# Optimization experiments

Hardware: AMD Instinct MI355X
Metric: run time of the kernel (lower is better)

The kernel has to match this reference:

```python
import jax, jax.numpy as jnp
import numpy as np

NUM_EXPERTS = 8
TOP_K = 2
HIDDEN = 1024
INTER = 1408


def setup_inputs() -> dict:
    key = jax.random.key(0)
    k0, k1, k2, k3, k4 = jax.random.split(key, 5)
    B, S = 2, 2048
    d_scale = HIDDEN ** -0.5
    i_scale = INTER ** -0.5
    return {
        "hidden_states": jax.random.normal(k0, (B, S, HIDDEN), jnp.float32),
        # nn.Linear(hidden, num_experts, bias=False): weight (E, d)
        "gate_w": jax.random.normal(k1, (NUM_EXPERTS, HIDDEN), jnp.float32) * d_scale,
        # per-expert SwiGLU weights, nn.Linear convention (out, in)
        "gate_proj": jax.random.normal(k2, (NUM_EXPERTS, INTER, HIDDEN), jnp.float32) * d_scale,
        "up_proj": jax.random.normal(k3, (NUM_EXPERTS, INTER, HIDDEN), jnp.float32) * d_scale,
        "down_proj": jax.random.normal(k4, (NUM_EXPERTS, HIDDEN, INTER), jnp.float32) * i_scale,
    }


def reference(hidden_states, gate_w, gate_proj, up_proj, down_proj):
    B, S, D = hidden_states.shape
    x = hidden_states.reshape(-1, D)  # (T, d)
    T = x.shape[0]

    # gate linear -> router logits (T, E)
    router_logits = x @ gate_w.T

    # TopKRouter: softmax in fp32 over all experts, top-k, optional renorm
    probs = jax.nn.softmax(router_logits.astype(jnp.float32), axis=-1)
    routing_weights, selected_experts = jax.lax.top_k(probs, TOP_K)  # (T, k)
    routing_weights = routing_weights / routing_weights.sum(axis=-1, keepdims=True)  # norm_topk_prob
    routing_weights = routing_weights.astype(x.dtype)

    # combine weights per (token, expert): scatter top-k weights into dense (T, E)
    combine = jnp.zeros((T, NUM_EXPERTS), x.dtype).at[
        jnp.arange(T)[:, None], selected_experts
    ].add(routing_weights)

    # per-expert SwiGLU FFN, weighted combine (loop over small fixed expert set)
    out = jnp.zeros_like(x)
    for e in range(NUM_EXPERTS):
        h = jax.nn.silu(x @ gate_proj[e].T) * (x @ up_proj[e].T)  # (T, i)
        out = out + combine[:, e : e + 1] * (h @ down_proj[e].T)  # (T, d)

    return out.reshape(B, S, D), router_logits
```

## Files before the change

kernel.cpp:

```cpp
#include <hip/hip_runtime.h>
#include <hip/hip_bf16.h>
#include <stdint.h>

#define T_TOK 4096
#define DH 1024
#define DI 1408
#define NE 8
#define TOPK 2
#define PADROWS 9216

typedef short s16x8 __attribute__((ext_vector_type(8)));
typedef float f32x4 __attribute__((ext_vector_type(4)));

__device__ inline unsigned f2bf(float f) {
    __hip_bfloat16 h = __float2bfloat16(f);
    return (unsigned)*(unsigned short*)&h;
}

__global__ __launch_bounds__(256) void cvt3_kernel(const float* __restrict__ s0,
        const float* __restrict__ s1, const float* __restrict__ s2,
        unsigned short* __restrict__ t0, unsigned short* __restrict__ t1,
        unsigned short* __restrict__ t2, int n4) {
    const float* src = blockIdx.y == 0 ? s0 : (blockIdx.y == 1 ? s1 : s2);
    unsigned short* dst = blockIdx.y == 0 ? t0 : (blockIdx.y == 1 ? t1 : t2);
    int i = blockIdx.x * blockDim.x + threadIdx.x;
    int stride = gridDim.x * blockDim.x;
    for (; i < n4; i += stride) {
        float4 v = ((const float4*)src)[i];
        uint2 o;
        o.x = f2bf(v.x) | (f2bf(v.y) << 16);
        o.y = f2bf(v.z) | (f2bf(v.w) << 16);
        ((uint2*)dst)[i] = o;
    }
}

__global__ __launch_bounds__(256) void router_kernel(const float* __restrict__ x,
                              const float* __restrict__ gw,
                              float* __restrict__ logits_out,
                              int* __restrict__ tokE, float* __restrict__ tokW,
                              unsigned short* __restrict__ xb) {
    int wave = threadIdx.x >> 6;
    int lane = threadIdx.x & 63;
    int t = blockIdx.x * 4 + wave;
    const float4* xr = (const float4*)(x + (size_t)t * DH);

    float acc[NE];
#pragma unroll
    for (int e = 0; e < NE; ++e) acc[e] = 0.f;

#pragma unroll
    for (int i = 0; i < 4; ++i) {
        float4 xv = xr[lane + i * 64];
#pragma unroll
        for (int e = 0; e < NE; ++e) {
            float4 g = ((const float4*)(gw + (size_t)e * DH))[lane + i * 64];
            acc[e] += xv.x * g.x + xv.y * g.y + xv.z * g.z + xv.w * g.w;
        }
        uint2 o;
        o.x = f2bf(xv.x) | (f2bf(xv.y) << 16);
        o.y = f2bf(xv.z) | (f2bf(xv.w) << 16);
        *(uint2*)(xb + (size_t)t * DH + (lane + i * 64) * 4) = o;
    }
#pragma unroll
    for (int e = 0; e < NE; ++e) {
#pragma unroll
        for (int off = 32; off > 0; off >>= 1) acc[e] += __shfl_xor(acc[e], off, 64);
    }
    if (lane == 0) {
        float mx = acc[0];
#pragma unroll
        for (int e = 1; e < NE; ++e) mx = fmaxf(mx, acc[e]);
        float p[NE]; float s = 0.f;
#pragma unroll
        for (int e = 0; e < NE; ++e) { p[e] = expf(acc[e] - mx); s += p[e]; }
        float inv = 1.f / s;
#pragma unroll
        for (int e = 0; e < NE; ++e) p[e] *= inv;
        int i0 = 0, i1 = -1; float p0 = -1.f, p1 = -1.f;
#pragma unroll
        for (int e = 0; e < NE; ++e) {
            float v = p[e];
            if (v > p0) { p1 = p0; i1 = i0; p0 = v; i0 = e; }
            else if (v > p1) { p1 = v; i1 = e; }
        }
        float wsum = p0 + p1;
#pragma unroll
        for (int e = 0; e < NE; ++e) logits_out[(size_t)t * NE + e] = acc[e];
        tokE[2 * t]     = i0;  tokE[2 * t + 1] = i1;
        tokW[2 * t]     = p0 / wsum;  tokW[2 * t + 1] = p1 / wsum;
    }
}

__global__ __launch_bounds__(256) void hist_kernel(const int* __restrict__ tokE,
        int* __restrict__ counts, int* __restrict__ padOff) {
    __shared__ int wc[4][NE];
    int tid = threadIdx.x;
    int wave = tid >> 6, lane = tid & 63;
    int cnt[NE];
#pragma unroll
    for (int e = 0; e < NE; ++e) cnt[e] = 0;
    for (int i = tid; i < T_TOK * TOPK; i += 256) {
        int v = tokE[i];
#pragma unroll
        for (int e = 0; e < NE; ++e)
            cnt[e] += (int)__popcll(__ballot(v == e));
    }
    if (lane == 0) {
#pragma unroll
        for (int e = 0; e < NE; ++e) wc[wave][e] = cnt[e];
    }
    __syncthreads();
    if (tid == 0) {
        int r = 0;
        for (int e = 0; e < NE; ++e) {
            int c = wc[0][e] + wc[1][e] + wc[2][e] + wc[3][e];
            counts[e] = c;
            padOff[e] = r;
            r += ((c + 127) >> 7) << 7;
        }
        padOff[NE] = r;
    }
}

__global__ __launch_bounds__(256) void scatter_kernel(const int* __restrict__ tokE,
                               const int* __restrict__ padOff, int* __restrict__ cursor,
                               int* __restrict__ assignTok, int* __restrict__ tokSlot) {
    int t = blockIdx.x * blockDim.x + threadIdx.x;
    int lane = threadIdx.x & 63;
    unsigned long long lmask = (1ull << lane) - 1ull;
#pragma unroll
    for (int k = 0; k < TOPK; ++k) {
        int e = tokE[2 * t + k];
#pragma unroll
        for (int ex = 0; ex < NE; ++ex) {
            unsigned long long m = __ballot(e == ex);
            if (e == ex) {
                int rank = (int)__popcll(m & lmask);
                int leader = __ffsll((long long)m) - 1;
                int b = 0;
                if (rank == 0) b = atomicAdd(&cursor[ex], (int)__popcll(m));
                b = __shfl(b, leader, 64);
                int slot = padOff[ex] + b + rank;
                assignTok[slot] = t;
                tokSlot[2 * t + k] = slot;
            }
        }
    }
}

__global__ __launch_bounds__(512) void gemmA_kernel(
        const unsigned short* __restrict__ xb,
        const unsigned short* __restrict__ gpb, const unsigned short* __restrict__ upb,
        const int* __restrict__ padOff, const int* __restrict__ assignTok,
        unsigned short* __restrict__ h) {
    int pr0 = blockIdx.y * 128;
    int e = -1;
#pragma unroll
    for (int i = 0; i < NE; ++i)
        if (pr0 >= padOff[i] && pr0 < padOff[i + 1]) e = i;
    if (e < 0) return;
    int n0 = blockIdx.x * 128;

    __shared__ unsigned short As[128 * 32];
    __shared__ unsigned short Bgs[128 * 32];
    __shared__ unsigned short Bus[128 * 32];

    int tid = threadIdx.x;
    int lane = tid & 63;
    int w = tid >> 6;
    int wm = (w >> 2) * 64;
    int wn = (w & 3) * 32;

    int tok = assignTok[pr0 + w * 16 + (lane >> 2)];
    const unsigned short* a_src = xb + (size_t)tok * DH + (lane & 3) * 8;
    unsigned short* a_dst = &As[w * 16 * 32];

    int brow = n0 + w * 16 + (lane >> 2);
    const unsigned short* g_src = gpb + ((size_t)e * DI + brow) * DH + (lane & 3) * 8;
    const unsigned short* u_src = upb + ((size_t)e * DI + brow) * DH + (lane & 3) * 8;
    unsigned short* bg_dst = &Bgs[w * 16 * 32];
    unsigned short* bu_dst = &Bus[w * 16 * 32];

    f32x4 accG[4][2], accU[4][2];
#pragma unroll
    for (int i = 0; i < 4; ++i)
#pragma unroll
        for (int j = 0; j < 2; ++j) {
            accG[i][j] = (f32x4){0.f, 0.f, 0.f, 0.f};
            accU[i][j] = (f32x4){0.f, 0.f, 0.f, 0.f};
        }

    for (int k0 = 0; k0 < DH; k0 += 32) {
        __builtin_amdgcn_global_load_lds(
            (const __attribute__((address_space(1))) void*)(a_src + k0),
            (__attribute__((address_space(3))) void*)a_dst, 16, 0, 0);
        __builtin_amdgcn_global_load_lds(
            (const __attribute__((address_space(1))) void*)(g_src + k0),
            (__attribute__((address_space(3))) void*)bg_dst, 16, 0, 0);
        __builtin_amdgcn_global_load_lds(
            (const __attribute__((address_space(1))) void*)(u_src + k0),
            (__attribute__((address_space(3))) void*)bu_dst, 16, 0, 0);
        __syncthreads();

        s16x8 af[4], bgf[2], buf_[2];
#pragma unroll
        for (int i = 0; i < 4; ++i)
            af[i] = *(const s16x8*)&As[(wm + 16 * i + (lane & 15)) * 32 + (lane >> 4) * 8];
#pragma unroll
        for (int j = 0; j < 2; ++j) {
            bgf[j]  = *(const s16x8*)&Bgs[(wn + 16 * j + (lane & 15)) * 32 + (lane >> 4) * 8];
            buf_[j] = *(const s16x8*)&Bus[(wn + 16 * j + (lane & 15)) * 32 + (lane >> 4) * 8];
        }
#pragma unroll
        for (int i = 0; i < 4; ++i)
#pragma unroll
            for (int j = 0; j < 2; ++j) {
                accG[i][j] = __builtin_amdgcn_mfma_f32_16x16x32_bf16(af[i], bgf[j], accG[i][j], 0, 0, 0);
                accU[i][j] = __builtin_amdgcn_mfma_f32_16x16x32_bf16(af[i], buf_[j], accU[i][j], 0, 0, 0);
            }
        __syncthreads();
    }

#pragma unroll
    for (int i = 0; i < 4; ++i) {
        int rowb = pr0 + wm + 16 * i + ((lane >> 4) << 2);
#pragma unroll
        for (int j = 0; j < 2; ++j) {
            int col = n0 + wn + 16 * j + (lane & 15);
#pragma unroll
            for (int r = 0; r < 4; ++r) {
                float g = accG[i][j][r], u = accU[i][j][r];
                float val = (g / (1.f + __expf(-g))) * u;
                h[(size_t)(rowb + r) * DI + col] = (unsigned short)f2bf(val);
            }
        }
    }
}

__global__ __launch_bounds__(512) void gemmB_kernel(
        const unsigned short* __restrict__ h,
        const unsigned short* __restrict__ dpb,
        const int* __restrict__ padOff, const int* __restrict__ counts,
        float* __restrict__ outP) {
    int pr0 = blockIdx.y * 128;
    int e = -1, base = 0;
#pragma unroll
    for (int i = 0; i < NE; ++i)
        if (pr0 >= padOff[i] && pr0 < padOff[i + 1]) { e = i; base = padOff[i]; }
    if (e < 0) return;
    int cnt = counts[e];
    int n0 = blockIdx.x * 128;

    __shared__ unsigned short As[128 * 32];
    __shared__ unsigned short Bs[128 * 32];

    int tid = threadIdx.x;
    int lane = tid & 63;
    int w = tid >> 6;
    int wm = (w >> 2) * 64;
    int wn = (w & 3) * 32;

    const unsigned short* a_src = h + (size_t)(pr0 + w * 16 + (lane >> 2)) * DI + (lane & 3) * 8;
    unsigned short* a_dst = &As[w * 16 * 32];

    int brow = n0 + w * 16 + (lane >> 2);
    const unsigned short* b_src = dpb + ((size_t)e * DH + brow) * DI + (lane & 3) * 8;
    unsigned short* b_dst = &Bs[w * 16 * 32];

    f32x4 acc[4][2];
#pragma unroll
    for (int i = 0; i < 4; ++i)
#pragma unroll
        for (int j = 0; j < 2; ++j) acc[i][j] = (f32x4){0.f, 0.f, 0.f, 0.f};

    for (int k0 = 0; k0 < DI; k0 += 32) {
        __builtin_amdgcn_global_load_lds(
            (const __attribute__((address_space(1))) void*)(a_src + k0),
            (__attribute__((address_space(3))) void*)a_dst, 16, 0, 0);
        __builtin_amdgcn_global_load_lds(
            (const __attribute__((address_space(1))) void*)(b_src + k0),
            (__attribute__((address_space(3))) void*)b_dst, 16, 0, 0);
        __syncthreads();

        s16x8 af[4], bf[2];
#pragma unroll
        for (int i = 0; i < 4; ++i)
            af[i] = *(const s16x8*)&As[(wm + 16 * i + (lane & 15)) * 32 + (lane >> 4) * 8];
#pragma unroll
        for (int j = 0; j < 2; ++j)
            bf[j] = *(const s16x8*)&Bs[(wn + 16 * j + (lane & 15)) * 32 + (lane >> 4) * 8];
#pragma unroll
        for (int i = 0; i < 4; ++i)
#pragma unroll
            for (int j = 0; j < 2; ++j)
                acc[i][j] = __builtin_amdgcn_mfma_f32_16x16x32_bf16(af[i], bf[j], acc[i][j], 0, 0, 0);
        __syncthreads();
    }

#pragma unroll
    for (int i = 0; i < 4; ++i) {
        int rowb = pr0 + wm + 16 * i + ((lane >> 4) << 2);
#pragma unroll
        for (int r = 0; r < 4; ++r) {
            int prow = rowb + r;
            if (prow - base < cnt) {
#pragma unroll
                for (int j = 0; j < 2; ++j) {
                    int col = n0 + wn + 16 * j + (lane & 15);
                    outP[(size_t)prow * DH + col] = acc[i][j][r];
                }
            }
        }
    }
}

__global__ __launch_bounds__(256) void combine_kernel(const float* __restrict__ outP,
        const int* __restrict__ tokSlot, const float* __restrict__ tokW,
        float* __restrict__ out) {
    int t = blockIdx.x;
    int c = threadIdx.x * 4;
    int s0 = tokSlot[2 * t], s1 = tokSlot[2 * t + 1];
    float w0 = tokW[2 * t], w1 = tokW[2 * t + 1];
    float4 a = *(const float4*)(outP + (size_t)s0 * DH + c);
    float4 b = *(const float4*)(outP + (size_t)s1 * DH + c);
    float4 o;
    o.x = w0 * a.x + w1 * b.x;
    o.y = w0 * a.y + w1 * b.y;
    o.z = w0 * a.z + w1 * b.z;
    o.w = w0 * a.w + w1 * b.w;
    *(float4*)(out + (size_t)t * DH + c) = o;
}

extern "C" void kernel_launch(void* const* d_in, const int* in_sizes, int n_in,
                              void* d_out, int out_size, void* d_ws, size_t ws_size,
                              hipStream_t stream) {
    const float* x  = (const float*)d_in[0];
    const float* gw = (const float*)d_in[1];
    const float* gp = (const float*)d_in[2];
    const float* up = (const float*)d_in[3];
    const float* dp = (const float*)d_in[4];
    float* out = (float*)d_out;
    float* logits = out + (size_t)T_TOK * DH;

    char* ws = (char*)d_ws;
    int*   counts    = (int*)(ws + 0);
    int*   cursor    = (int*)(ws + 64);
    int*   padOff    = (int*)(ws + 128);
    int*   tokE      = (int*)(ws + 4096);
    float* tokW      = (float*)(ws + 36864);
    int*   tokSlot   = (int*)(ws + 69632);
    int*   assignTok = (int*)(ws + 102400);
    unsigned short* xb  = (unsigned short*)(ws + 139264);
    unsigned short* gpb = (unsigned short*)(ws + 8527872);
    unsigned short* upb = (unsigned short*)(ws + 31596544);
    unsigned short* dpb = (unsigned short*)(ws + 54665216);
    unsigned short* h   = (unsigned short*)(ws + 77733888);
    float* outP = (float*)(ws + 8527872);

    hipMemsetAsync(ws, 0, 256, stream);
    hipMemsetAsync(ws + 102400, 0, PADROWS * 4, stream);

    const int NW4 = NE * DI * DH / 4;
    cvt3_kernel<<<dim3(1024, 3), 256, 0, stream>>>(gp, up, dp, gpb, upb, dpb, NW4);

    router_kernel<<<T_TOK / 4, 256, 0, stream>>>(x, gw, logits, tokE, tokW, xb);
    hist_kernel<<<1, 256, 0, stream>>>(tokE, counts, padOff);
    scatter_kernel<<<T_TOK / 256, 256, 0, stream>>>(tokE, padOff, cursor, assignTok, tokSlot);

    gemmA_kernel<<<dim3(DI / 128, PADROWS / 128), 512, 0, stream>>>(xb, gpb, upb, padOff, assignTok, h);
    gemmB_kernel<<<dim3(DH / 128, PADROWS / 128), 512, 0, stream>>>(h, dpb, padOff, counts, outP);
    combine_kernel<<<T_TOK, 256, 0, stream>>>(outP, tokSlot, tokW, out);
}
```

Baseline: 224.6 us.

## Double-buffer LDS and enlarge row tiles to 256 in MoE expert GEMMs

Both expert GEMMs now use 256-row tiles (expert padding raised to 256) with double-buffered LDS, so the global-to-LDS copies for the next K slice are issued while MFMAs run on the current one. The launch becomes a flat 1D grid whose block index is remapped by an XCD-style permutation to spread tiles across dies. The intent is to hide load latency, reuse each weight tile across more rows, and halve the barriers per K step. In exchange it roughly doubles accumulator registers and LDS per block, and more blocks compute padding rows.

```diff
diff --git a/kernel.cpp b/kernel.cpp
--- a/kernel.cpp
+++ b/kernel.cpp
@@ -7,7 +7,7 @@
 #define DI 1408
 #define NE 8
 #define TOPK 2
-#define PADROWS 9216
+#define PADROWS 10240
 
 typedef short s16x8 __attribute__((ext_vector_type(8)));
 typedef float f32x4 __attribute__((ext_vector_type(4)));
@@ -16,6 +16,10 @@
     __hip_bfloat16 h = __float2bfloat16(f);
     return (unsigned)*(unsigned short*)&h;
 }
+
+#define GLDS(src, dst) __builtin_amdgcn_global_load_lds( \
+    (const __attribute__((address_space(1))) void*)(src), \
+    (__attribute__((address_space(3))) void*)(dst), 16, 0, 0)
 
 __global__ __launch_bounds__(256) void cvt3_kernel(const float* __restrict__ s0,
         const float* __restrict__ s1, const float* __restrict__ s2,
@@ -116,7 +120,7 @@
             int c = wc[0][e] + wc[1][e] + wc[2][e] + wc[3][e];
             counts[e] = c;
             padOff[e] = r;
-            r += ((c + 127) >> 7) << 7;
+            r += ((c + 255) >> 8) << 8;
         }
         padOff[NE] = r;
     }
@@ -153,66 +157,69 @@
         const unsigned short* __restrict__ gpb, const unsigned short* __restrict__ upb,
         const int* __restrict__ padOff, const int* __restrict__ assignTok,
         unsigned short* __restrict__ h) {
-    int pr0 = blockIdx.y * 128;
+    int bid = blockIdx.x;
+    int nid = (bid & 7) * 55 + (bid >> 3);
+    int colblk = nid / 40, rowblk = nid - colblk * 40;
+    int pr0 = rowblk * 256;
+    int n0 = colblk * 128;
     int e = -1;
 #pragma unroll
     for (int i = 0; i < NE; ++i)
         if (pr0 >= padOff[i] && pr0 < padOff[i + 1]) e = i;
     if (e < 0) return;
-    int n0 = blockIdx.x * 128;
-
-    __shared__ unsigned short As[128 * 32];
-    __shared__ unsigned short Bgs[128 * 32];
-    __shared__ unsigned short Bus[128 * 32];
+
+    __shared__ unsigned short As[2][256 * 32];
+    __shared__ unsigned short Bgs[2][128 * 32];
+    __shared__ unsigned short Bus[2][128 * 32];
 
     int tid = threadIdx.x;
     int lane = tid & 63;
     int w = tid >> 6;
-    int wm = (w >> 2) * 64;
+    int wm = (w >> 2) * 128;
     int wn = (w & 3) * 32;
 
-    int tok = assignTok[pr0 + w * 16 + (lane >> 2)];
-    const unsigned short* a_src = xb + (size_t)tok * DH + (lane & 3) * 8;
-    unsigned short* a_dst = &As[w * 16 * 32];
-
-    int brow = n0 + w * 16 + (lane >> 2);
-    const unsigned short* g_src = gpb + ((size_t)e * DI + brow) * DH + (lane & 3) * 8;
-    const unsigned short* u_src = upb + ((size_t)e * DI + brow) * DH + (lane & 3) * 8;
-    unsigned short* bg_dst = &Bgs[w * 16 * 32];
-    unsigned short* bu_dst = &Bus[w * 16 * 32];
-
-    f32x4 accG[4][2], accU[4][2];
-#pragma unroll
-    for (int i = 0; i < 4; ++i)
+    int tok0 = assignTok[pr0 + w * 16 + (lane >> 2)];
+    int tok1 = assignTok[pr0 + 128 + w * 16 + (lane >> 2)];
+    const unsigned short* a0 = xb + (size_t)tok0 * DH + (lane & 3) * 8;
+    const unsigned short* a1 = xb + (size_t)tok1 * DH + (lane & 3) * 8;
+    int brow = n0 + (tid >> 2);
+    const unsigned short* gsrc = gpb + ((size_t)e * DI + brow) * DH + (tid & 3) * 8;
+    const unsigned short* usrc = upb + ((size_t)e * DI + brow) * DH + (tid & 3) * 8;
+
+    f32x4 accG[8][2], accU[8][2];
+#pragma unroll
+    for (int i = 0; i < 8; ++i)
 #pragma unroll
         for (int j = 0; j < 2; ++j) {
             accG[i][j] = (f32x4){0.f, 0.f, 0.f, 0.f};
             accU[i][j] = (f32x4){0.f, 0.f, 0.f, 0.f};
         }
 
-    for (int k0 = 0; k0 < DH; k0 += 32) {
-        __builtin_amdgcn_global_load_lds(
-            (const __attribute__((address_space(1))) void*)(a_src + k0),
-            (__attribute__((address_space(3))) void*)a_dst, 16, 0, 0);
-        __builtin_amdgcn_global_load_lds(
-            (const __attribute__((address_space(1))) void*)(g_src + k0),
-            (__attribute__((address_space(3))) void*)bg_dst, 16, 0, 0);
-        __builtin_amdgcn_global_load_lds(
-            (const __attribute__((address_space(1))) void*)(u_src + k0),
-            (__attribute__((address_space(3))) void*)bu_dst, 16, 0, 0);
-        __syncthreads();
-
-        s16x8 af[4], bgf[2], buf_[2];
-#pragma unroll
-        for (int i = 0; i < 4; ++i)
-            af[i] = *(const s16x8*)&As[(wm + 16 * i + (lane & 15)) * 32 + (lane >> 4) * 8];
+#define STAGE_A(buf, k0) do { \
+    GLDS(a0 + (k0),   &As[buf][w * 512]); \
+    GLDS(a1 + (k0),   &As[buf][4096 + w * 512]); \
+    GLDS(gsrc + (k0), &Bgs[buf][w * 512]); \
+    GLDS(usrc + (k0), &Bus[buf][w * 512]); \
+    } while (0)
+
+    STAGE_A(0, 0);
+    __syncthreads();
+
+    for (int ks = 0; ks < 32; ++ks) {
+        int cur = ks & 1;
+        if (ks < 31) STAGE_A(cur ^ 1, (ks + 1) * 32);
+
+        s16x8 af[8], bgf[2], buf_[2];
+#pragma unroll
+        for (int i = 0; i < 8; ++i)
+            af[i] = *(const s16x8*)&As[cur][(wm + 16 * i + (lane & 15)) * 32 + (lane >> 4) * 8];
 #pragma unroll
         for (int j = 0; j < 2; ++j) {
-            bgf[j]  = *(const s16x8*)&Bgs[(wn + 16 * j + (lane & 15)) * 32 + (lane >> 4) * 8];
-            buf_[j] = *(const s16x8*)&Bus[(wn + 16 * j + (lane & 15)) * 32 + (lane >> 4) * 8];
-        }
-#pragma unroll
-        for (int i = 0; i < 4; ++i)
+            bgf[j]  = *(const s16x8*)&Bgs[cur][(wn + 16 * j + (lane & 15)) * 32 + (lane >> 4) * 8];
+            buf_[j] = *(const s16x8*)&Bus[cur][(wn + 16 * j + (lane & 15)) * 32 + (lane >> 4) * 8];
+        }
+#pragma unroll
+        for (int i = 0; i < 8; ++i)
 #pragma unroll
             for (int j = 0; j < 2; ++j) {
                 accG[i][j] = __builtin_amdgcn_mfma_f32_16x16x32_bf16(af[i], bgf[j], accG[i][j], 0, 0, 0);
@@ -220,9 +227,10 @@
             }
         __syncthreads();
     }
-
-#pragma unroll
-    for (int i = 0; i < 4; ++i) {
+#undef STAGE_A
+
+#pragma unroll
+    for (int i = 0; i < 8; ++i) {
         int rowb = pr0 + wm + 16 * i + ((lane >> 4) << 2);
 #pragma unroll
         for (int j = 0; j < 2; ++j) {
@@ -242,63 +250,69 @@
         const unsigned short* __restrict__ dpb,
         const int* __restrict__ padOff, const int* __restrict__ counts,
         float* __restrict__ outP) {
-    int pr0 = blockIdx.y * 128;
+    int bid = blockIdx.x;
+    int nid = (bid & 7) * 40 + (bid >> 3);
+    int colblk = nid / 40, rowblk = nid - colblk * 40;
+    int pr0 = rowblk * 256;
+    int n0 = colblk * 128;
     int e = -1, base = 0;
 #pragma unroll
     for (int i = 0; i < NE; ++i)
         if (pr0 >= padOff[i] && pr0 < padOff[i + 1]) { e = i; base = padOff[i]; }
     if (e < 0) return;
     int cnt = counts[e];
-    int n0 = blockIdx.x * 128;
-
-    __shared__ unsigned short As[128 * 32];
-    __shared__ unsigned short Bs[128 * 32];
+
+    __shared__ unsigned short As[2][256 * 32];
+    __shared__ unsigned short Bs[2][128 * 32];
 
     int tid = threadIdx.x;
     int lane = tid & 63;
     int w = tid >> 6;
-    int wm = (w >> 2) * 64;
+    int wm = (w >> 2) * 128;
     int wn = (w & 3) * 32;
 
-    const unsigned short* a_src = h + (size_t)(pr0 + w * 16 + (lane >> 2)) * DI + (lane & 3) * 8;
-    unsigned short* a_dst = &As[w * 16 * 32];
-
-    int brow = n0 + w * 16 + (lane >> 2);
-    const unsigned short* b_src = dpb + ((size_t)e * DH + brow) * DI + (lane & 3) * 8;
-    unsigned short* b_dst = &Bs[w * 16 * 32];
-
-    f32x4 acc[4][2];
-#pragma unroll
-    for (int i = 0; i < 4; ++i)
+    const unsigned short* a0 = h + (size_t)(pr0 + w * 16 + (lane >> 2)) * DI + (lane & 3) * 8;
+    const unsigned short* a1 = h + (size_t)(pr0 + 128 + w * 16 + (lane >> 2)) * DI + (lane & 3) * 8;
+    int brow = n0 + (tid >> 2);
+    const unsigned short* bsrc = dpb + ((size_t)e * DH + brow) * DI + (tid & 3) * 8;
+
+    f32x4 acc[8][2];
+#pragma unroll
+    for (int i = 0; i < 8; ++i)
 #pragma unroll
         for (int j = 0; j < 2; ++j) acc[i][j] = (f32x4){0.f, 0.f, 0.f, 0.f};
 
-    for (int k0 = 0; k0 < DI; k0 += 32) {
-        __builtin_amdgcn_global_load_lds(
-            (const __attribute__((address_space(1))) void*)(a_src + k0),
-            (__attribute__((address_space(3))) void*)a_dst, 16, 0, 0);
-        __builtin_amdgcn_global_load_lds(
-            (const __attribute__((address_space(1))) void*)(b_src + k0),
-            (__attribute__((address_space(3))) void*)b_dst, 16, 0, 0);
-        __syncthreads();
-
-        s16x8 af[4], bf[2];
-#pragma unroll
-        for (int i = 0; i < 4; ++i)
-            af[i] = *(const s16x8*)&As[(wm + 16 * i + (lane & 15)) * 32 + (lane >> 4) * 8];
+#define STAGE_B(buf, k0) do { \
+    GLDS(a0 + (k0),   &As[buf][w * 512]); \
+    GLDS(a1 + (k0),   &As[buf][4096 + w * 512]); \
+    GLDS(bsrc + (k0), &Bs[buf][w * 512]); \
+    } while (0)
+
+    STAGE_B(0, 0);
+    __syncthreads();
+
+    for (int ks = 0; ks < 44; ++ks) {
+        int cur = ks & 1;
+        if (ks < 43) STAGE_B(cur ^ 1, (ks + 1) * 32);
+
+        s16x8 af[8], bf[2];
+#pragma unroll
+        for (int i = 0; i < 8; ++i)
+            af[i] = *(const s16x8*)&As[cur][(wm + 16 * i + (lane & 15)) * 32 + (lane >> 4) * 8];
 #pragma unroll
         for (int j = 0; j < 2; ++j)
-            bf[j] = *(const s16x8*)&Bs[(wn + 16 * j + (lane & 15)) * 32 + (lane >> 4) * 8];
-#pragma unroll
-        for (int i = 0; i < 4; ++i)
+            bf[j] = *(const s16x8*)&Bs[cur][(wn + 16 * j + (lane & 15)) * 32 + (lane >> 4) * 8];
+#pragma unroll
+        for (int i = 0; i < 8; ++i)
 #pragma unroll
             for (int j = 0; j < 2; ++j)
                 acc[i][j] = __builtin_amdgcn_mfma_f32_16x16x32_bf16(af[i], bf[j], acc[i][j], 0, 0, 0);
         __syncthreads();
     }
-
-#pragma unroll
-    for (int i = 0; i < 4; ++i) {
+#undef STAGE_B
+
+#pragma unroll
+    for (int i = 0; i < 8; ++i) {
         int rowb = pr0 + wm + 16 * i + ((lane >> 4) << 2);
 #pragma unroll
         for (int r = 0; r < 4; ++r) {
@@ -350,12 +364,12 @@
     float* tokW      = (float*)(ws + 36864);
     int*   tokSlot   = (int*)(ws + 69632);
     int*   assignTok = (int*)(ws + 102400);
-    unsigned short* xb  = (unsigned short*)(ws + 139264);
-    unsigned short* gpb = (unsigned short*)(ws + 8527872);
-    unsigned short* upb = (unsigned short*)(ws + 31596544);
-    unsigned short* dpb = (unsigned short*)(ws + 54665216);
-    unsigned short* h   = (unsigned short*)(ws + 77733888);
-    float* outP = (float*)(ws + 8527872);
+    unsigned short* xb  = (unsigned short*)(ws + 147456);
+    unsigned short* gpb = (unsigned short*)(ws + 8536064);
+    unsigned short* upb = (unsigned short*)(ws + 31604736);
+    unsigned short* dpb = (unsigned short*)(ws + 54673408);
+    unsigned short* h   = (unsigned short*)(ws + 77742080);
+    float* outP = (float*)(ws + 8536064);
 
     hipMemsetAsync(ws, 0, 256, stream);
     hipMemsetAsync(ws + 102400, 0, PADROWS * 4, stream);
@@ -367,7 +381,7 @@
     hist_kernel<<<1, 256, 0, stream>>>(tokE, counts, padOff);
     scatter_kernel<<<T_TOK / 256, 256, 0, stream>>>(tokE, padOff, cursor, assignTok, tokSlot);
 
-    gemmA_kernel<<<dim3(DI / 128, PADROWS / 128), 512, 0, stream>>>(xb, gpb, upb, padOff, assignTok, h);
-    gemmB_kernel<<<dim3(DH / 128, PADROWS / 128), 512, 0, stream>>>(h, dpb, padOff, counts, outP);
+    gemmA_kernel<<<dim3((DI / 128) * (PADROWS / 256)), 512, 0, stream>>>(xb, gpb, upb, padOff, assignTok, h);
+    gemmB_kernel<<<dim3((DH / 128) * (PADROWS / 256)), 512, 0, stream>>>(h, dpb, padOff, counts, outP);
     combine_kernel<<<T_TOK, 256, 0, stream>>>(outP, tokSlot, tokW, out);
 }
```

Result: slower. 239.4 us (+6.6%).
